# Kernel tuning notes

Measured on AMD Instinct MI355X. Metric: run time of the kernel, lower is better.

Reference implementation:

```python
import jax, jax.numpy as jnp
import numpy as np

N = 100000   # nodes
E = 1600000  # edges
IN, H, OUT = 128, 128, 40
BN_EPS = 1e-5


def setup_inputs() -> dict:
    key = jax.random.key(0)
    ks = jax.random.split(key, 8)
    x = jax.random.normal(ks[0], (N, IN), jnp.float32)
    edge_src = jax.random.randint(ks[1], (E,), 0, N, jnp.int32)
    edge_dst = jax.random.randint(ks[2], (E,), 0, N, jnp.int32)

    def glorot(k, shape):
        lim = (6.0 / (shape[0] + shape[1])) ** 0.5
        return jax.random.uniform(k, shape, jnp.float32, -lim, lim)

    return {
        "x": x, "edge_src": edge_src, "edge_dst": edge_dst,
        "W1": glorot(ks[3], (IN, H)), "b1": jnp.zeros((H,), jnp.float32),
        "g1": jnp.ones((H,), jnp.float32), "bt1": jnp.zeros((H,), jnp.float32),
        "W2": glorot(ks[4], (H, H)), "b2": jnp.zeros((H,), jnp.float32),
        "g2": jnp.ones((H,), jnp.float32), "bt2": jnp.zeros((H,), jnp.float32),
        "Wr": glorot(ks[5], (H, OUT)), "br": jnp.zeros((OUT,), jnp.float32),
    }


def _gcn_conv(h_in, W, b, src, dst, dinv):
    # GCNConv: D^{-1/2}(A+I)D^{-1/2} X W + b  (symmetric norm w/ self-loops)
    h = h_in @ W                                   # [N,H]
    coef = dinv[src] * dinv[dst]                   # [E]
    agg = jax.ops.segment_sum(h[src] * coef[:, None], dst, num_segments=N)
    agg = agg + h * (dinv * dinv)[:, None]         # self-loop contribution
    return agg + b


def _bn_relu(h, gamma, beta):
    # BatchNorm1d in training mode (batch stats, biased variance) + ReLU
    mean = jnp.mean(h, axis=0)
    var = jnp.var(h, axis=0)
    y = (h - mean) * jax.lax.rsqrt(var + BN_EPS) * gamma + beta
    return jax.nn.relu(y)


def reference(x, edge_src, edge_dst, W1, b1, g1, bt1, W2, b2, g2, bt2, Wr, br):
    ones = jnp.ones((E,), jnp.float32)
    deg = jax.ops.segment_sum(ones, edge_dst, num_segments=N) + 1.0  # +1 self-loop
    dinv = jax.lax.rsqrt(deg)

    h = _gcn_conv(x, W1, b1, edge_src, edge_dst, dinv)
    h = _bn_relu(h, g1, bt1)
    h = _gcn_conv(h, W2, b2, edge_src, edge_dst, dinv)
    h = _bn_relu(h, g2, bt2)
    # dropout omitted (deterministic eval); readout linear
    return h @ Wr + br
```

## Files before the change

kernel.cpp:

```cpp
#include <hip/hip_runtime.h>
#include <hip/hip_bf16.h>
#include <hip/hip_fp16.h>

#define H_DIM 128

typedef _Float16 half8 __attribute__((ext_vector_type(8)));
typedef float floatx4 __attribute__((ext_vector_type(4)));

__device__ inline int imax(int a, int b) { return a > b ? a : b; }
__device__ inline int imin(int a, int b) { return a < b ? a : b; }

__global__ void degree_kernel(const int* __restrict__ dst, int* __restrict__ deg, int E_) {
    int i = blockIdx.x * blockDim.x + threadIdx.x;
    if (i < E_) atomicAdd(&deg[dst[i]], 1);
}

__global__ void scan_block_kernel(const int* __restrict__ deg, float* __restrict__ dinv,
                                  int* __restrict__ rowptr, int* __restrict__ bsum, int N_) {
    __shared__ int sh[256];
    int i = blockIdx.x * 256 + threadIdx.x;
    int v = (i < N_) ? deg[i] : 0;
    if (i < N_) dinv[i] = rsqrtf((float)v + 1.0f);
    int pd = (i < N_) ? imax(24, (v + 7) & ~7) : 0;
    sh[threadIdx.x] = pd;
    __syncthreads();
    for (int off = 1; off < 256; off <<= 1) {
        int t = (threadIdx.x >= off) ? sh[threadIdx.x - off] : 0;
        __syncthreads();
        sh[threadIdx.x] += t;
        __syncthreads();
    }
    if (i < N_) rowptr[i] = sh[threadIdx.x] - pd;
    if (threadIdx.x == 255) bsum[blockIdx.x] = sh[255];
}

__global__ void scan_add_kernel(int* __restrict__ rowptr, const int* __restrict__ bsum,
                                const int* __restrict__ deg, int* __restrict__ cols, int N_,
                                float2* __restrict__ zrowA, float2* __restrict__ zrowB) {
    __shared__ int red[256];
    const int b = blockIdx.x, t = threadIdx.x;
    if (b == 0 && t < 32) {
        zrowA[t] = make_float2(0.f, 0.f);
        zrowB[t] = make_float2(0.f, 0.f);
    }
    int s = 0;
    for (int j = t; j < b; j += 256) s += bsum[j];
    red[t] = s;
    __syncthreads();
    for (int off = 128; off > 0; off >>= 1) {
        if (t < off) red[t] += red[t + off];
        __syncthreads();
    }
    int boff = red[0];
    int i = b * 256 + t;
    if (i < N_) {
        int start = rowptr[i] + boff;
        rowptr[i] = start;
        int d = deg[i];
        int pd = imax(24, (d + 7) & ~7);
        int padv = N_ << 8;
        for (int j = start + d; j < start + pd; ++j) cols[j] = padv;
        if (i == N_ - 1) rowptr[N_] = start + pd;
    }
}

__global__ void csr_fill_kernel(const int* __restrict__ src, const int* __restrict__ dst,
                                const int* __restrict__ rowptr, int* __restrict__ cursor,
                                int* __restrict__ cols, int E_, int N_, int shift) {
    int b = blockIdx.x & 7;
    if (((N_ - 1) >> shift) < b) return;
    int i = (blockIdx.x >> 3) * blockDim.x + threadIdx.x;
    if (i < E_) {
        int d = dst[i];
        if ((d >> shift) == b) {
            int p = rowptr[d] + atomicAdd(&cursor[d], 1);
            cols[p] = src[i] << 8;
        }
    }
}

__device__ inline half8 a_frag_f32(const float* Xr, int k0) {
    float4 v0 = *(const float4*)(Xr + k0);
    float4 v1 = *(const float4*)(Xr + k0 + 4);
    half8 a;
    a[0] = (_Float16)v0.x; a[1] = (_Float16)v0.y; a[2] = (_Float16)v0.z; a[3] = (_Float16)v0.w;
    a[4] = (_Float16)v1.x; a[5] = (_Float16)v1.y; a[6] = (_Float16)v1.z; a[7] = (_Float16)v1.w;
    return a;
}
__device__ inline half8 a_frag_f16_bn(const _Float16* Xr, int k0,
                                      const float* A, const float* B) {
    half8 r = *(const half8*)(Xr + k0);
    float4 a0 = *(const float4*)(A + k0);
    float4 a1 = *(const float4*)(A + k0 + 4);
    float4 b0 = *(const float4*)(B + k0);
    float4 b1 = *(const float4*)(B + k0 + 4);
    half8 o;
    o[0] = (_Float16)fmaxf(fmaf((float)r[0], a0.x, b0.x), 0.f);
    o[1] = (_Float16)fmaxf(fmaf((float)r[1], a0.y, b0.y), 0.f);
    o[2] = (_Float16)fmaxf(fmaf((float)r[2], a0.z, b0.z), 0.f);
    o[3] = (_Float16)fmaxf(fmaf((float)r[3], a0.w, b0.w), 0.f);
    o[4] = (_Float16)fmaxf(fmaf((float)r[4], a1.x, b1.x), 0.f);
    o[5] = (_Float16)fmaxf(fmaf((float)r[5], a1.y, b1.y), 0.f);
    o[6] = (_Float16)fmaxf(fmaf((float)r[6], a1.z, b1.z), 0.f);
    o[7] = (_Float16)fmaxf(fmaf((float)r[7], a1.w, b1.w), 0.f);
    return o;
}

template<bool BN, typename InT>
__global__ __launch_bounds__(256) void gemm_mfma_kernel(
    const InT* __restrict__ X, const float* __restrict__ W,
    const float* __restrict__ gsum, const float* __restrict__ gsq,
    const float* __restrict__ gamma, const float* __restrict__ beta,
    const float* __restrict__ dinv,
    _Float16* __restrict__ Y, int N_)
{
    __shared__ _Float16 Wf[32 * 64 * 8];
    __shared__ __align__(16) float Alds[128], Blds[128];

    const int tid = threadIdx.x;
    if constexpr (BN) {
        if (tid < 128) {
            float inv_n = 1.0f / (float)N_;
            float mean = gsum[tid] * inv_n;
            float var  = gsq[tid] * inv_n - mean * mean;
            float a = rsqrtf(var + 1e-5f) * gamma[tid];
            Alds[tid] = a;
            Blds[tid] = beta[tid] - mean * a;
        }
    }
    for (int idx = tid; idx < 128 * 32; idx += 256) {
        int k = idx >> 5;
        int n0 = (idx & 31) * 4;
        float4 w = *(const float4*)(W + k * 128 + n0);
        int kb = k >> 5, q = (k >> 3) & 3, j = k & 7;
#pragma unroll
        for (int u = 0; u < 4; ++u) {
            int n = n0 + u;
            int lane = (n & 15) | (q << 4);
            Wf[((((n >> 4) * 4 + kb) * 64 + lane) << 3) + j] = (_Float16)((&w.x)[u]);
        }
    }
    __syncthreads();

    const int wv = tid >> 6, lane = tid & 63;
    const int m = lane & 15, q = lane >> 4;
    const int row0 = blockIdx.x * 64 + wv * 16;

    int arow = row0 + m;
    if (arow >= N_) arow = N_ - 1;
    const InT* Xr = X + (size_t)arow * H_DIM;

    half8 a[4];
#pragma unroll
    for (int kb = 0; kb < 4; ++kb) {
        int k0 = kb * 32 + q * 8;
        if constexpr (BN) a[kb] = a_frag_f16_bn((const _Float16*)Xr, k0, Alds, Blds);
        else              a[kb] = a_frag_f32((const float*)Xr, k0);
    }

    floatx4 acc[8];
#pragma unroll
    for (int nt = 0; nt < 8; ++nt) acc[nt] = (floatx4){0.f, 0.f, 0.f, 0.f};

#pragma unroll
    for (int nt = 0; nt < 8; ++nt) {
#pragma unroll
        for (int kb = 0; kb < 4; ++kb) {
            half8 b = *(const half8*)&Wf[(((nt * 4 + kb) * 64 + lane) << 3)];
            acc[nt] = __builtin_amdgcn_mfma_f32_16x16x32_f16(a[kb], b, acc[nt], 0, 0, 0);
        }
    }

#pragma unroll
    for (int r = 0; r < 4; ++r) {
        int row = row0 + q * 4 + r;
        if (row < N_) {
            float ds = dinv[row];
            _Float16* Yr = Y + (size_t)row * H_DIM + m;
#pragma unroll
            for (int nt = 0; nt < 8; ++nt)
                Yr[nt * 16] = (_Float16)(ds * acc[nt][r]);
        }
    }
}

__global__ __launch_bounds__(256) void readout_mfma_kernel(
    const _Float16* __restrict__ X, const float* __restrict__ W,
    const float* __restrict__ gsum, const float* __restrict__ gsq,
    const float* __restrict__ gamma, const float* __restrict__ beta,
    const float* __restrict__ br,
    float* __restrict__ Y, int N_, int OUTC)
{
    __shared__ _Float16 Wf[12 * 64 * 8];
    __shared__ __align__(16) float Alds[128], Blds[128];

    const int tid = threadIdx.x;
    if (tid < 128) {
        float inv_n = 1.0f / (float)N_;
        float mean = gsum[tid] * inv_n;
        float var  = gsq[tid] * inv_n - mean * mean;
        float a = rsqrtf(var + 1e-5f) * gamma[tid];
        Alds[tid] = a;
        Blds[tid] = beta[tid] - mean * a;
    }
    for (int idx = tid; idx < 128 * 64; idx += 256) {
        int k = idx >> 6, n = idx & 63;
        if (n < 48) {
            float w = (n < OUTC) ? W[k * OUTC + n] : 0.f;
            int kb = k >> 5, q = (k >> 3) & 3, j = k & 7;
            int lane = (n & 15) | (q << 4);
            Wf[((((n >> 4) * 4 + kb) * 64 + lane) << 3) + j] = (_Float16)w;
        }
    }
    __syncthreads();

    const int wv = tid >> 6, lane = tid & 63;
    const int m = lane & 15, q = lane >> 4;
    const int row0 = blockIdx.x * 64 + wv * 16;

    int arow = row0 + m;
    if (arow >= N_) arow = N_ - 1;
    const _Float16* Xr = X + (size_t)arow * H_DIM;

    half8 a[4];
#pragma unroll
    for (int kb = 0; kb < 4; ++kb)
        a[kb] = a_frag_f16_bn(Xr, kb * 32 + q * 8, Alds, Blds);

    floatx4 acc[3];
#pragma unroll
    for (int nt = 0; nt < 3; ++nt) acc[nt] = (floatx4){0.f, 0.f, 0.f, 0.f};

#pragma unroll
    for (int nt = 0; nt < 3; ++nt) {
#pragma unroll
        for (int kb = 0; kb < 4; ++kb) {
            half8 b = *(const half8*)&Wf[(((nt * 4 + kb) * 64 + lane) << 3)];
            acc[nt] = __builtin_amdgcn_mfma_f32_16x16x32_f16(a[kb], b, acc[nt], 0, 0, 0);
        }
    }

#pragma unroll
    for (int nt = 0; nt < 3; ++nt) {
        int col = nt * 16 + m;
        if (col < OUTC) {
            float bb = br[col];
#pragma unroll
            for (int r = 0; r < 4; ++r) {
                int row = row0 + q * 4 + r;
                if (row < N_)
                    Y[(size_t)row * OUTC + col] = acc[nt][r] + bb;
            }
        }
    }
}

__global__ __launch_bounds__(256) void aggregate_stats_kernel(
    const __half2* __restrict__ Gp,
    const int* __restrict__ rowptr,
    const int* __restrict__ cols,
    const float* __restrict__ dinv, const float* __restrict__ bias,
    __half2* __restrict__ out,
    float* __restrict__ gsum, float* __restrict__ gsq,
    int N_, int stride)
{
    const int wave = threadIdx.x >> 6;
    const int lane = threadIdx.x & 63;
    const int c2 = lane * 2;
    const float bs0 = bias[c2], bs1 = bias[c2 + 1];
    const char* gpb = (const char*)Gp;
    const unsigned lane4 = (unsigned)lane * 4u;
    const __half2 z = __float2half2_rn(0.f);

    float r0 = 0.f, r1 = 0.f, q0 = 0.f, q1 = 0.f;

    const int n0 = blockIdx.x * 4 + wave;
    int e0 = 0, e1 = 0, f0 = 0, f1 = 0;
    int c[24];
    if (n0 < N_) {
        e0 = __builtin_amdgcn_readfirstlane(rowptr[n0]);
        e1 = __builtin_amdgcn_readfirstlane(rowptr[n0 + 1]);
        int n1 = n0 + stride; if (n1 > N_ - 1) n1 = N_ - 1;
        f0 = __builtin_amdgcn_readfirstlane(rowptr[n1]);
        f1 = __builtin_amdgcn_readfirstlane(rowptr[n1 + 1]);
#pragma unroll
        for (int u = 0; u < 24; ++u) c[u] = cols[e0 + u];
    }

    for (int n = n0; n < N_; n += stride) {
        __half2 self = *(const __half2*)(gpb + (((unsigned)n << 8) + lane4));
        __half2 h[24];
#pragma unroll
        for (int u = 0; u < 24; ++u)
            h[u] = *(const __half2*)(gpb + ((unsigned)c[u] + lane4));

        int n2 = n + 2 * stride; if (n2 > N_ - 1) n2 = N_ - 1;
        int g0 = __builtin_amdgcn_readfirstlane(rowptr[n2]);
        int g1 = __builtin_amdgcn_readfirstlane(rowptr[n2 + 1]);

#pragma unroll
        for (int u = 0; u < 24; ++u) c[u] = cols[f0 + u];

        __half2 acc[8];
        acc[0] = self;
#pragma unroll
        for (int u = 1; u < 8; ++u) acc[u] = z;
#pragma unroll
        for (int u = 0; u < 24; ++u)
            acc[u & 7] = __hadd2(acc[u & 7], h[u]);

        for (int e = e0 + 24; e < e1; e += 8) {
            __half2 t[8];
#pragma unroll
            for (int u = 0; u < 8; ++u)
                t[u] = *(const __half2*)(gpb + ((unsigned)cols[e + u] + lane4));
#pragma unroll
            for (int u = 0; u < 8; ++u) acc[u] = __hadd2(acc[u], t[u]);
        }

        __half2 p0 = __hadd2(__hadd2(acc[0], acc[1]), __hadd2(acc[2], acc[3]));
        __half2 p1 = __hadd2(__hadd2(acc[4], acc[5]), __hadd2(acc[6], acc[7]));
        float2 F0 = __half22float2(p0);
        float2 F1 = __half22float2(p1);
        float di = dinv[n];
        float o0 = fmaf(di, F0.x + F1.x, bs0);
        float o1 = fmaf(di, F0.y + F1.y, bs1);
        out[((size_t)n << 6) + lane] = __floats2half2_rn(o0, o1);

        r0 += o0; r1 += o1;
        q0 = fmaf(o0, o0, q0); q1 = fmaf(o1, o1, q1);

        e0 = f0; e1 = f1; f0 = g0; f1 = g1;
    }

    __shared__ float ssum[4][128], ssq[4][128];
    ssum[wave][c2] = r0; ssum[wave][c2 + 1] = r1;
    ssq[wave][c2]  = q0; ssq[wave][c2 + 1]  = q1;
    __syncthreads();
    if (threadIdx.x < 128) {
        int k = threadIdx.x;
        float s = (ssum[0][k] + ssum[1][k]) + (ssum[2][k] + ssum[3][k]);
        float q = (ssq[0][k] + ssq[1][k]) + (ssq[2][k] + ssq[3][k]);
        atomicAdd(&gsum[k], s);
        atomicAdd(&gsq[k], q);
    }
}

extern "C" void kernel_launch(void* const* d_in, const int* in_sizes, int n_in,
                              void* d_out, int out_size, void* d_ws, size_t ws_size,
                              hipStream_t stream) {
    const float* x   = (const float*)d_in[0];
    const int* esrc  = (const int*)d_in[1];
    const int* edst  = (const int*)d_in[2];
    const float* W1  = (const float*)d_in[3];
    const float* b1  = (const float*)d_in[4];
    const float* g1  = (const float*)d_in[5];
    const float* bt1 = (const float*)d_in[6];
    const float* W2  = (const float*)d_in[7];
    const float* b2  = (const float*)d_in[8];
    const float* g2  = (const float*)d_in[9];
    const float* bt2 = (const float*)d_in[10];
    const float* Wr  = (const float*)d_in[11];
    const float* br  = (const float*)d_in[12];

    const int N_ = in_sizes[0] / H_DIM;
    const int E_ = in_sizes[1];
    const int OUTC = out_size / N_;

    char* p = (char*)d_ws;
    auto alloc = [&](size_t bytes) -> void* {
        void* r = (void*)p;
        p += (bytes + 255) & ~(size_t)255;
        return r;
    };
    __half* tmpA = (__half*)alloc((size_t)(N_ + 1) * H_DIM * 2);
    __half* tmpB = (__half*)alloc((size_t)(N_ + 1) * H_DIM * 2);
    int*   cols  = (int*)  alloc(((size_t)E_ + 31 * (size_t)N_ + 64) * 4);
    int*   rowptr= (int*)  alloc((size_t)(N_ + 1) * 4);
    size_t degcur_sz = ((size_t)2 * N_ * 4 + 255) & ~(size_t)255;
    int*   degcur= (int*)  alloc((size_t)2 * N_ * 4);
    float* bnbuf = (float*)alloc(8 * 128 * 4);
    int*   deg   = degcur;
    int*   cursor= degcur + N_;
    float* sum1 = bnbuf,       *sq1 = bnbuf + 128;
    float* sum2 = bnbuf + 256, *sq2 = bnbuf + 384;
    float* dinv  = (float*)alloc((size_t)N_ * 4);
    int*   bsum  = (int*)  alloc(4096);

    hipMemsetAsync(degcur, 0, degcur_sz + 4 * 128 * 4, stream);

    const int nb = (N_ + 255) / 256;
    const int eb = (E_ + 255) / 256;
    const int ntiles64 = (N_ + 63) / 64;

    int shift = 0;
    while (((N_ - 1) >> shift) > 7) ++shift;

    const int AGG_BLOCKS = 2048;
    const int AGG_STRIDE = AGG_BLOCKS * 4;

    degree_kernel<<<eb, 256, 0, stream>>>(edst, deg, E_);
    scan_block_kernel<<<nb, 256, 0, stream>>>(deg, dinv, rowptr, bsum, N_);
    scan_add_kernel<<<nb, 256, 0, stream>>>(rowptr, bsum, deg, cols, N_,
        (float2*)(tmpA + (size_t)N_ * H_DIM), (float2*)(tmpB + (size_t)N_ * H_DIM));
    csr_fill_kernel<<<eb * 8, 256, 0, stream>>>(esrc, edst, rowptr, cursor, cols, E_, N_, shift);

    gemm_mfma_kernel<false, float><<<ntiles64, 256, 0, stream>>>(
        x, W1, nullptr, nullptr, nullptr, nullptr, dinv, (_Float16*)tmpA, N_);
    aggregate_stats_kernel<<<AGG_BLOCKS, 256, 0, stream>>>(
        (const __half2*)tmpA, rowptr, cols, dinv, b1, (__half2*)tmpB,
        sum1, sq1, N_, AGG_STRIDE);

    gemm_mfma_kernel<true, _Float16><<<ntiles64, 256, 0, stream>>>(
        (const _Float16*)tmpB, W2, sum1, sq1, g1, bt1, dinv, (_Float16*)tmpA, N_);
    aggregate_stats_kernel<<<AGG_BLOCKS, 256, 0, stream>>>(
        (const __half2*)tmpA, rowptr, cols, dinv, b2, (__half2*)tmpB,
        sum2, sq2, N_, AGG_STRIDE);

    readout_mfma_kernel<<<ntiles64, 256, 0, stream>>>(
        (const _Float16*)tmpB, Wr, sum2, sq2, g2, bt2, br, (float*)d_out, N_, OUTC);
}
```

Before: 507.7 us.

## Pre-bin edges by destination range before CSR fill to avoid redundant scans

Result: slower. 616.5 us (+21.4%).

```diff
diff --git a/kernel.cpp b/kernel.cpp
--- a/kernel.cpp
+++ b/kernel.cpp
@@ -10,13 +10,26 @@
 __device__ inline int imax(int a, int b) { return a > b ? a : b; }
 __device__ inline int imin(int a, int b) { return a < b ? a : b; }
 
-__global__ void degree_kernel(const int* __restrict__ dst, int* __restrict__ deg, int E_) {
-    int i = blockIdx.x * blockDim.x + threadIdx.x;
-    if (i < E_) atomicAdd(&deg[dst[i]], 1);
+__global__ void degree_kernel(const int* __restrict__ dst, int* __restrict__ deg,
+                              int* __restrict__ bcnt, int E_, int shift) {
+    __shared__ int lb[8];
+    const int tid = threadIdx.x;
+    if (tid < 8) lb[tid] = 0;
+    __syncthreads();
+    int i = blockIdx.x * blockDim.x + tid;
+    if (i < E_) {
+        int d = dst[i];
+        atomicAdd(&deg[d], 1);
+        atomicAdd(&lb[d >> shift], 1);
+    }
+    __syncthreads();
+    if (tid < 8 && lb[tid]) atomicAdd(&bcnt[tid], lb[tid]);
 }
 
 __global__ void scan_block_kernel(const int* __restrict__ deg, float* __restrict__ dinv,
-                                  int* __restrict__ rowptr, int* __restrict__ bsum, int N_) {
+                                  int* __restrict__ rowptr, int* __restrict__ bsum,
+                                  const int* __restrict__ bcnt, int* __restrict__ bbase,
+                                  int* __restrict__ bcur, int N_) {
     __shared__ int sh[256];
     int i = blockIdx.x * 256 + threadIdx.x;
     int v = (i < N_) ? deg[i] : 0;
@@ -32,6 +45,11 @@
     }
     if (i < N_) rowptr[i] = sh[threadIdx.x] - pd;
     if (threadIdx.x == 255) bsum[blockIdx.x] = sh[255];
+    if (blockIdx.x == 0 && threadIdx.x == 0) {
+        int s = 0;
+#pragma unroll
+        for (int k = 0; k < 8; ++k) { bbase[k] = s; bcur[k] = s; s += bcnt[k]; }
+    }
 }
 
 __global__ void scan_add_kernel(int* __restrict__ rowptr, const int* __restrict__ bsum,
@@ -64,18 +82,38 @@
     }
 }
 
-__global__ void csr_fill_kernel(const int* __restrict__ src, const int* __restrict__ dst,
-                                const int* __restrict__ rowptr, int* __restrict__ cursor,
-                                int* __restrict__ cols, int E_, int N_, int shift) {
+__global__ void bin_edges_kernel(const int* __restrict__ src, const int* __restrict__ dst,
+                                 int2* __restrict__ pairs, int* __restrict__ bcur,
+                                 int E_, int shift) {
+    __shared__ int lcnt[8], lbase[8];
+    const int tid = threadIdx.x;
+    if (tid < 8) lcnt[tid] = 0;
+    __syncthreads();
+    int i = blockIdx.x * 256 + tid;
+    int d = 0, b = 0, pos = 0;
+    if (i < E_) {
+        d = dst[i];
+        b = d >> shift;
+        pos = atomicAdd(&lcnt[b], 1);
+    }
+    __syncthreads();
+    if (tid < 8 && lcnt[tid]) lbase[tid] = atomicAdd(&bcur[tid], lcnt[tid]);
+    __syncthreads();
+    if (i < E_) {
+        int2 pr; pr.x = src[i] << 8; pr.y = d;
+        pairs[lbase[b] + pos] = pr;
+    }
+}
+
+__global__ void csr_fill_kernel(const int2* __restrict__ pairs, const int* __restrict__ bbase,
+                                const int* __restrict__ bcnt, const int* __restrict__ rowptr,
+                                int* __restrict__ cursor, int* __restrict__ cols) {
     int b = blockIdx.x & 7;
-    if (((N_ - 1) >> shift) < b) return;
-    int i = (blockIdx.x >> 3) * blockDim.x + threadIdx.x;
-    if (i < E_) {
-        int d = dst[i];
-        if ((d >> shift) == b) {
-            int p = rowptr[d] + atomicAdd(&cursor[d], 1);
-            cols[p] = src[i] << 8;
-        }
+    int j = (blockIdx.x >> 3) * 256 + threadIdx.x;
+    if (j < bcnt[b]) {
+        int2 pr = pairs[bbase[b] + j];
+        int p = rowptr[pr.y] + atomicAdd(&cursor[pr.y], 1);
+        cols[p] = pr.x;
     }
 }
 
@@ -377,6 +415,7 @@
     __half* tmpB = (__half*)alloc((size_t)(N_ + 1) * H_DIM * 2);
     int*   cols  = (int*)  alloc(((size_t)E_ + 31 * (size_t)N_ + 64) * 4);
     int*   rowptr= (int*)  alloc((size_t)(N_ + 1) * 4);
+    int2*  pairs = (int2*) alloc((size_t)E_ * 8);
     size_t degcur_sz = ((size_t)2 * N_ * 4 + 255) & ~(size_t)255;
     int*   degcur= (int*)  alloc((size_t)2 * N_ * 4);
     float* bnbuf = (float*)alloc(8 * 128 * 4);
@@ -384,10 +423,13 @@
     int*   cursor= degcur + N_;
     float* sum1 = bnbuf,       *sq1 = bnbuf + 128;
     float* sum2 = bnbuf + 256, *sq2 = bnbuf + 384;
+    int*   bcnt  = (int*)(bnbuf + 512);
+    int*   bbase = (int*)(bnbuf + 520);
+    int*   bcur  = (int*)(bnbuf + 528);
     float* dinv  = (float*)alloc((size_t)N_ * 4);
     int*   bsum  = (int*)  alloc(4096);
 
-    hipMemsetAsync(degcur, 0, degcur_sz + 4 * 128 * 4, stream);
+    hipMemsetAsync(degcur, 0, degcur_sz + 544 * 4, stream);
 
     const int nb = (N_ + 255) / 256;
     const int eb = (E_ + 255) / 256;
@@ -399,11 +441,12 @@
     const int AGG_BLOCKS = 2048;
     const int AGG_STRIDE = AGG_BLOCKS * 4;
 
-    degree_kernel<<<eb, 256, 0, stream>>>(edst, deg, E_);
-    scan_block_kernel<<<nb, 256, 0, stream>>>(deg, dinv, rowptr, bsum, N_);
+    degree_kernel<<<eb, 256, 0, stream>>>(edst, deg, bcnt, E_, shift);
+    scan_block_kernel<<<nb, 256, 0, stream>>>(deg, dinv, rowptr, bsum, bcnt, bbase, bcur, N_);
     scan_add_kernel<<<nb, 256, 0, stream>>>(rowptr, bsum, deg, cols, N_,
         (float2*)(tmpA + (size_t)N_ * H_DIM), (float2*)(tmpB + (size_t)N_ * H_DIM));
-    csr_fill_kernel<<<eb * 8, 256, 0, stream>>>(esrc, edst, rowptr, cursor, cols, E_, N_, shift);
+    bin_edges_kernel<<<eb, 256, 0, stream>>>(esrc, edst, pairs, bcur, E_, shift);
+    csr_fill_kernel<<<eb * 8, 256, 0, stream>>>(pairs, bbase, bcnt, rowptr, cursor, cols);
 
     gemm_mfma_kernel<false, float><<<ntiles64, 256, 0, stream>>>(
         x, W1, nullptr, nullptr, nullptr, nullptr, dinv, (_Float16*)tmpA, N_);
```
